# Optimization experiments

Hardware: AMD Instinct MI355X
Metric: run time of the kernel (lower is better)

Reference implementation:

```python
import jax, jax.numpy as jnp
import numpy as np

N, D_IN, D_OUT = 8192, 256, 64
NEG_INF = -9e15
LEAKY_SLOPE = 0.2  # tf.nn.leaky_relu default alpha


def setup_inputs() -> dict:
    key = jax.random.key(0)
    k1, k2, k3, k4 = jax.random.split(key, 4)
    x = jax.random.normal(k1, (N, D_IN), dtype=jnp.float32)
    adj = jax.random.randint(k2, (N, N), 0, 2, dtype=jnp.int32)
    W = jax.random.normal(k3, (D_IN, D_OUT), dtype=jnp.float32) * (1.0 / np.sqrt(D_IN))
    a = jax.random.normal(k4, (2 * D_OUT, 1), dtype=jnp.float32) * (1.0 / np.sqrt(2 * D_OUT))
    b = jnp.zeros((D_OUT,), dtype=jnp.float32)
    return {"x": x, "adj": adj, "W": W, "a": a, "b": b}


def reference(x, adj, W, a, b):
    # z: [N, D_OUT]
    z = x @ W
    # Additive GAT scores: e[i,j] = leaky_relu(a1.z_i + a2.z_j)
    # (equivalent to the tile/concat + matmul with a in the original,
    #  but avoids the [N*N, 2D] intermediate)
    a1 = a[:D_OUT, 0]   # [D_OUT]
    a2 = a[D_OUT:, 0]   # [D_OUT]
    si = z @ a1         # [N]
    sj = z @ a2         # [N]
    e = jax.nn.leaky_relu(si[:, None] + sj[None, :], negative_slope=LEAKY_SLOPE)
    masked = jnp.where(adj > 0, e, NEG_INF)
    alpha = jax.nn.softmax(masked, axis=1)  # row-wise over neighbors
    out = alpha @ z + b
    return jax.nn.relu(out)
```

## Files before the change

### kernel.cpp

```cpp
#include <hip/hip_runtime.h>
#include <hip/hip_bf16.h>

#define N 8192
#define DIN 256
#define DOUT 64
#define JSPLIT 16
#define JSPAN (N / JSPLIT)
#define NITILES (N / 64)
#define LEAKY 0.2f

typedef __attribute__((ext_vector_type(8))) short bf16x8;
typedef __attribute__((ext_vector_type(4))) float f32x4;

#define OFF_ZT   ((size_t)0)
#define OFF_SI   (OFF_ZT + (size_t)DOUT * N * 2)
#define OFF_SJ   (OFF_SI + (size_t)N * 4)
#define OFF_MAX  (OFF_SJ + (size_t)N * 4)
#define OFF_PDEN (OFF_MAX + 256)
#define OFF_PNUM (OFF_PDEN + (size_t)JSPLIT * N * 4)

static __device__ __forceinline__ short f2bf(float f) {
  union { __hip_bfloat16 h; short s; } u;
  u.h = __float2bfloat16(f);
  return u.s;
}

static __device__ __forceinline__ unsigned fkey(float f) {
  int b = __float_as_int(f);
  return (b < 0) ? ~(unsigned)b : ((unsigned)b | 0x80000000u);
}
static __device__ __forceinline__ float fdec(unsigned k) {
  int b = (k & 0x80000000u) ? (int)(k & 0x7fffffffu) : (int)~k;
  return __int_as_float(b);
}

__global__ __launch_bounds__(256) void gat_proj(
    const float* __restrict__ x, const float* __restrict__ W,
    const float* __restrict__ a, __hip_bfloat16* __restrict__ zT,
    float* __restrict__ si, float* __restrict__ sj,
    unsigned* __restrict__ mx) {
  __shared__ float wmx[4][2];
  const int lane = threadIdx.x & 63;
  const int wave = threadIdx.x >> 6;
  const int rowbase = blockIdx.x * 16 + wave * 4;
  float acc[4] = {0.f, 0.f, 0.f, 0.f};
  for (int k = 0; k < DIN; k += 4) {
    const float w0 = W[(k + 0) * DOUT + lane];
    const float w1 = W[(k + 1) * DOUT + lane];
    const float w2 = W[(k + 2) * DOUT + lane];
    const float w3 = W[(k + 3) * DOUT + lane];
#pragma unroll
    for (int r = 0; r < 4; ++r) {
      const float4 xv = *reinterpret_cast<const float4*>(&x[(size_t)(rowbase + r) * DIN + k]);
      acc[r] += xv.x * w0 + xv.y * w1 + xv.z * w2 + xv.w * w3;
    }
  }
  const float a1l = a[lane];
  const float a2l = a[DOUT + lane];
  float wm1 = -1e30f, wm2 = -1e30f;
#pragma unroll
  for (int r = 0; r < 4; ++r) {
    const int row = rowbase + r;
    zT[(size_t)lane * N + row] = __float2bfloat16(acc[r]);
    float v1 = acc[r] * a1l;
    float v2 = acc[r] * a2l;
#pragma unroll
    for (int m = 1; m < 64; m <<= 1) {
      v1 += __shfl_xor(v1, m);
      v2 += __shfl_xor(v2, m);
    }
    if (lane == 0) { si[row] = v1; sj[row] = v2; }
    wm1 = fmaxf(wm1, v1);
    wm2 = fmaxf(wm2, v2);
  }
  if (lane == 0) { wmx[wave][0] = wm1; wmx[wave][1] = wm2; }
  __syncthreads();
  if (threadIdx.x == 0) {
    float M1 = fmaxf(fmaxf(wmx[0][0], wmx[1][0]), fmaxf(wmx[2][0], wmx[3][0]));
    float M2 = fmaxf(fmaxf(wmx[0][1], wmx[1][1]), fmaxf(wmx[2][1], wmx[3][1]));
    atomicMax(mx + 0, fkey(M1));
    atomicMax(mx + 1, fkey(M2));
  }
}

__global__ __launch_bounds__(256, 6) void gat_main(
    const int* __restrict__ adj, const float* __restrict__ si,
    const float* __restrict__ sj, const __hip_bfloat16* __restrict__ zT,
    const unsigned* __restrict__ mx, float* __restrict__ pnum,
    float* __restrict__ pden) {
  const int lane = threadIdx.x & 63;
  const int wave = threadIdx.x >> 6;
  const int itile = blockIdx.x % NITILES;
  const int jchunk = blockIdx.x / NITILES;
  const int r16 = lane & 15;
  const int kgrp = lane >> 4;
  const int row = itile * 64 + wave * 16 + r16;
  const int jbase = jchunk * JSPAN;

  unsigned bm0 = 0, bm1 = 0, bm2 = 0, bm3 = 0;
  {
    const int* __restrict__ abase =
        adj + (size_t)(itile * 64 + wave * 16) * N + jbase;
#pragma unroll 1
    for (int rr = 0; rr < 16; ++rr) {
      const int* __restrict__ ar = abase + (size_t)rr * N;
#pragma unroll
      for (int w = 0; w < 8; ++w) {
        const int v = ar[w * 64 + lane];
        const unsigned long long m = __ballot(v > 0);
        const unsigned byte0 = (unsigned)(m >> (kgrp * 8)) & 0xffu;
        const unsigned byte1 = (unsigned)(m >> (32 + kgrp * 8)) & 0xffu;
        const unsigned contrib = (byte0 | (byte1 << 8)) << ((w & 1) * 16);
        if (r16 == rr) {
          if ((w >> 1) == 0) bm0 |= contrib;
          else if ((w >> 1) == 1) bm1 |= contrib;
          else if ((w >> 1) == 2) bm2 |= contrib;
          else bm3 |= contrib;
        }
      }
    }
  }

  const float tC = fdec(mx[0]) + fdec(mx[1]);
  const float C = tC > 0.f ? tC : LEAKY * tC;
  const float sir = si[row];

  const float* __restrict__ sp = sj + jbase + kgrp * 8;
  const __hip_bfloat16* __restrict__ zb0 = zT + (size_t)r16 * N + jbase + kgrp * 8;
  const __hip_bfloat16* __restrict__ zb1 = zb0 + (size_t)16 * N;
  const __hip_bfloat16* __restrict__ zb2 = zb0 + (size_t)32 * N;
  const __hip_bfloat16* __restrict__ zb3 = zb0 + (size_t)48 * N;

  f32x4 acc0 = {0.f, 0.f, 0.f, 0.f};
  f32x4 acc1 = acc0, acc2 = acc0, acc3 = acc0;
  float dacc = 0.f;

#pragma unroll
  for (int ph = 0; ph < 4; ++ph) {
    const unsigned bmp = (ph == 0) ? bm0 : (ph == 1) ? bm1 : (ph == 2) ? bm2 : bm3;
#pragma unroll
    for (int sub = 0; sub < 4; ++sub) {
      const int it = ph * 4 + sub;
      const unsigned bits = (bmp >> (sub * 8)) & 0xffu;

      const bf16x8 b0 = *reinterpret_cast<const bf16x8*>(zb0 + it * 32);
      const bf16x8 b1 = *reinterpret_cast<const bf16x8*>(zb1 + it * 32);
      const bf16x8 b2 = *reinterpret_cast<const bf16x8*>(zb2 + it * 32);
      const bf16x8 b3 = *reinterpret_cast<const bf16x8*>(zb3 + it * 32);
      const float4 s0 = *reinterpret_cast<const float4*>(sp + it * 32);
      const float4 s1 = *reinterpret_cast<const float4*>(sp + it * 32 + 4);

      float p0, p1, p2, p3, p4, p5, p6, p7, t;
      t = sir + s0.x; t = fmaxf(t, LEAKY * t); p0 = (bits & 1u)   ? __expf(t - C) : 0.f;
      t = sir + s0.y; t = fmaxf(t, LEAKY * t); p1 = (bits & 2u)   ? __expf(t - C) : 0.f;
      t = sir + s0.z; t = fmaxf(t, LEAKY * t); p2 = (bits & 4u)   ? __expf(t - C) : 0.f;
      t = sir + s0.w; t = fmaxf(t, LEAKY * t); p3 = (bits & 8u)   ? __expf(t - C) : 0.f;
      t = sir + s1.x; t = fmaxf(t, LEAKY * t); p4 = (bits & 16u)  ? __expf(t - C) : 0.f;
      t = sir + s1.y; t = fmaxf(t, LEAKY * t); p5 = (bits & 32u)  ? __expf(t - C) : 0.f;
      t = sir + s1.z; t = fmaxf(t, LEAKY * t); p6 = (bits & 64u)  ? __expf(t - C) : 0.f;
      t = sir + s1.w; t = fmaxf(t, LEAKY * t); p7 = (bits & 128u) ? __expf(t - C) : 0.f;

      dacc += ((p0 + p1) + (p2 + p3)) + ((p4 + p5) + (p6 + p7));

      bf16x8 afr;
      afr[0] = f2bf(p0); afr[1] = f2bf(p1); afr[2] = f2bf(p2); afr[3] = f2bf(p3);
      afr[4] = f2bf(p4); afr[5] = f2bf(p5); afr[6] = f2bf(p6); afr[7] = f2bf(p7);

      acc0 = __builtin_amdgcn_mfma_f32_16x16x32_bf16(afr, b0, acc0, 0, 0, 0);
      acc1 = __builtin_amdgcn_mfma_f32_16x16x32_bf16(afr, b1, acc1, 0, 0, 0);
      acc2 = __builtin_amdgcn_mfma_f32_16x16x32_bf16(afr, b2, acc2, 0, 0, 0);
      acc3 = __builtin_amdgcn_mfma_f32_16x16x32_bf16(afr, b3, acc3, 0, 0, 0);
    }
  }

  dacc += __shfl_xor(dacc, 16);
  dacc += __shfl_xor(dacc, 32);
  if (lane < 16) pden[(size_t)jchunk * N + row] = dacc;

  float* np = pnum + ((size_t)jchunk * N + (size_t)itile * 64 + wave * 16) * DOUT;
  const f32x4 accs[4] = {acc0, acc1, acc2, acc3};
#pragma unroll
  for (int dt = 0; dt < 4; ++dt) {
#pragma unroll
    for (int r = 0; r < 4; ++r) {
      np[(kgrp * 4 + r) * DOUT + dt * 16 + r16] = accs[dt][r];
    }
  }
}

__global__ __launch_bounds__(256) void gat_combine(
    const float* __restrict__ pnum, const float* __restrict__ pden,
    const float* __restrict__ b, float* __restrict__ out) {
  const int idx = blockIdx.x * 256 + threadIdx.x;
  const int row = idx >> 6;
  const int d = idx & 63;
  float num = 0.f, den = 0.f;
#pragma unroll
  for (int s = 0; s < JSPLIT; ++s) num += pnum[(size_t)s * N * DOUT + idx];
#pragma unroll
  for (int s = 0; s < JSPLIT; ++s) den += pden[(size_t)s * N + row];
  const float o = num / den + b[d];
  out[idx] = o > 0.f ? o : 0.f;
}

extern "C" void kernel_launch(void* const* d_in, const int* in_sizes, int n_in,
                              void* d_out, int out_size, void* d_ws, size_t ws_size,
                              hipStream_t stream) {
  const float* x = (const float*)d_in[0];
  const int* adj = (const int*)d_in[1];
  const float* W = (const float*)d_in[2];
  const float* a = (const float*)d_in[3];
  const float* b = (const float*)d_in[4];
  float* out = (float*)d_out;
  char* ws = (char*)d_ws;

  __hip_bfloat16* zT = (__hip_bfloat16*)(ws + OFF_ZT);
  float* si = (float*)(ws + OFF_SI);
  float* sj = (float*)(ws + OFF_SJ);
  unsigned* mx = (unsigned*)(ws + OFF_MAX);
  float* pden = (float*)(ws + OFF_PDEN);
  float* pnum = (float*)(ws + OFF_PNUM);

  gat_proj<<<dim3(N / 16), dim3(256), 0, stream>>>(x, W, a, zT, si, sj, mx);
  gat_main<<<dim3(NITILES * JSPLIT), dim3(256), 0, stream>>>(adj, si, sj, zT, mx,
                                                             pnum, pden);
  gat_combine<<<dim3((N * DOUT) / 256), dim3(256), 0, stream>>>(pnum, pden, b, out);
}
```

Baseline: 480.9 us.

## Stage z tile in LDS and split j range into 32 chunks

```diff
diff --git a/kernel.cpp b/kernel.cpp
--- a/kernel.cpp
+++ b/kernel.cpp
@@ -4,8 +4,9 @@
 #define N 8192
 #define DIN 256
 #define DOUT 64
-#define JSPLIT 16
+#define JSPLIT 32
 #define JSPAN (N / JSPLIT)
+#define KSTEPS (JSPAN / 32)
 #define NITILES (N / 64)
 #define LEAKY 0.2f
 
@@ -83,13 +84,15 @@
   }
 }
 
-__global__ __launch_bounds__(256, 6) void gat_main(
+__global__ __launch_bounds__(256, 4) void gat_main(
     const int* __restrict__ adj, const float* __restrict__ si,
     const float* __restrict__ sj, const __hip_bfloat16* __restrict__ zT,
     const unsigned* __restrict__ mx, float* __restrict__ pnum,
     float* __restrict__ pden) {
-  const int lane = threadIdx.x & 63;
-  const int wave = threadIdx.x >> 6;
+  __shared__ short lds_z[64][264];
+  const int tid = threadIdx.x;
+  const int lane = tid & 63;
+  const int wave = tid >> 6;
   const int itile = blockIdx.x % NITILES;
   const int jchunk = blockIdx.x / NITILES;
   const int r16 = lane & 15;
@@ -97,80 +100,81 @@
   const int row = itile * 64 + wave * 16 + r16;
   const int jbase = jchunk * JSPAN;
 
-  unsigned bm0 = 0, bm1 = 0, bm2 = 0, bm3 = 0;
+  {
+    const int r = tid >> 5;
+    const int cb = (tid & 31) * 8;
+#pragma unroll
+    for (int rr = 0; rr < 8; ++rr) {
+      const int d = rr * 8 + r;
+      const bf16x8 v =
+          *reinterpret_cast<const bf16x8*>(zT + (size_t)d * N + jbase + cb);
+      *reinterpret_cast<bf16x8*>(&lds_z[d][cb]) = v;
+    }
+  }
+
+  unsigned bm0 = 0, bm1 = 0;
   {
     const int* __restrict__ abase =
         adj + (size_t)(itile * 64 + wave * 16) * N + jbase;
-#pragma unroll 1
+#pragma unroll
     for (int rr = 0; rr < 16; ++rr) {
-      const int* __restrict__ ar = abase + (size_t)rr * N;
-#pragma unroll
-      for (int w = 0; w < 8; ++w) {
-        const int v = ar[w * 64 + lane];
+#pragma unroll
+      for (int w = 0; w < 4; ++w) {
+        const int v = abase[(size_t)rr * N + w * 64 + lane];
         const unsigned long long m = __ballot(v > 0);
         const unsigned byte0 = (unsigned)(m >> (kgrp * 8)) & 0xffu;
         const unsigned byte1 = (unsigned)(m >> (32 + kgrp * 8)) & 0xffu;
         const unsigned contrib = (byte0 | (byte1 << 8)) << ((w & 1) * 16);
         if (r16 == rr) {
-          if ((w >> 1) == 0) bm0 |= contrib;
-          else if ((w >> 1) == 1) bm1 |= contrib;
-          else if ((w >> 1) == 2) bm2 |= contrib;
-          else bm3 |= contrib;
+          if (w < 2) bm0 |= contrib; else bm1 |= contrib;
         }
       }
     }
   }
+  __syncthreads();
 
   const float tC = fdec(mx[0]) + fdec(mx[1]);
   const float C = tC > 0.f ? tC : LEAKY * tC;
   const float sir = si[row];
-
   const float* __restrict__ sp = sj + jbase + kgrp * 8;
-  const __hip_bfloat16* __restrict__ zb0 = zT + (size_t)r16 * N + jbase + kgrp * 8;
-  const __hip_bfloat16* __restrict__ zb1 = zb0 + (size_t)16 * N;
-  const __hip_bfloat16* __restrict__ zb2 = zb0 + (size_t)32 * N;
-  const __hip_bfloat16* __restrict__ zb3 = zb0 + (size_t)48 * N;
 
   f32x4 acc0 = {0.f, 0.f, 0.f, 0.f};
   f32x4 acc1 = acc0, acc2 = acc0, acc3 = acc0;
   float dacc = 0.f;
 
 #pragma unroll
-  for (int ph = 0; ph < 4; ++ph) {
-    const unsigned bmp = (ph == 0) ? bm0 : (ph == 1) ? bm1 : (ph == 2) ? bm2 : bm3;
-#pragma unroll
-    for (int sub = 0; sub < 4; ++sub) {
-      const int it = ph * 4 + sub;
-      const unsigned bits = (bmp >> (sub * 8)) & 0xffu;
-
-      const bf16x8 b0 = *reinterpret_cast<const bf16x8*>(zb0 + it * 32);
-      const bf16x8 b1 = *reinterpret_cast<const bf16x8*>(zb1 + it * 32);
-      const bf16x8 b2 = *reinterpret_cast<const bf16x8*>(zb2 + it * 32);
-      const bf16x8 b3 = *reinterpret_cast<const bf16x8*>(zb3 + it * 32);
-      const float4 s0 = *reinterpret_cast<const float4*>(sp + it * 32);
-      const float4 s1 = *reinterpret_cast<const float4*>(sp + it * 32 + 4);
-
-      float p0, p1, p2, p3, p4, p5, p6, p7, t;
-      t = sir + s0.x; t = fmaxf(t, LEAKY * t); p0 = (bits & 1u)   ? __expf(t - C) : 0.f;
-      t = sir + s0.y; t = fmaxf(t, LEAKY * t); p1 = (bits & 2u)   ? __expf(t - C) : 0.f;
-      t = sir + s0.z; t = fmaxf(t, LEAKY * t); p2 = (bits & 4u)   ? __expf(t - C) : 0.f;
-      t = sir + s0.w; t = fmaxf(t, LEAKY * t); p3 = (bits & 8u)   ? __expf(t - C) : 0.f;
-      t = sir + s1.x; t = fmaxf(t, LEAKY * t); p4 = (bits & 16u)  ? __expf(t - C) : 0.f;
-      t = sir + s1.y; t = fmaxf(t, LEAKY * t); p5 = (bits & 32u)  ? __expf(t - C) : 0.f;
-      t = sir + s1.z; t = fmaxf(t, LEAKY * t); p6 = (bits & 64u)  ? __expf(t - C) : 0.f;
-      t = sir + s1.w; t = fmaxf(t, LEAKY * t); p7 = (bits & 128u) ? __expf(t - C) : 0.f;
-
-      dacc += ((p0 + p1) + (p2 + p3)) + ((p4 + p5) + (p6 + p7));
-
-      bf16x8 afr;
-      afr[0] = f2bf(p0); afr[1] = f2bf(p1); afr[2] = f2bf(p2); afr[3] = f2bf(p3);
-      afr[4] = f2bf(p4); afr[5] = f2bf(p5); afr[6] = f2bf(p6); afr[7] = f2bf(p7);
-
-      acc0 = __builtin_amdgcn_mfma_f32_16x16x32_bf16(afr, b0, acc0, 0, 0, 0);
-      acc1 = __builtin_amdgcn_mfma_f32_16x16x32_bf16(afr, b1, acc1, 0, 0, 0);
-      acc2 = __builtin_amdgcn_mfma_f32_16x16x32_bf16(afr, b2, acc2, 0, 0, 0);
-      acc3 = __builtin_amdgcn_mfma_f32_16x16x32_bf16(afr, b3, acc3, 0, 0, 0);
-    }
+  for (int it = 0; it < KSTEPS; ++it) {
+    const unsigned bmp = (it < 4) ? bm0 : bm1;
+    const unsigned bits = (bmp >> ((it & 3) * 8)) & 0xffu;
+    const int col = it * 32 + kgrp * 8;
+
+    const bf16x8 b0 = *reinterpret_cast<const bf16x8*>(&lds_z[r16][col]);
+    const bf16x8 b1 = *reinterpret_cast<const bf16x8*>(&lds_z[16 + r16][col]);
+    const bf16x8 b2 = *reinterpret_cast<const bf16x8*>(&lds_z[32 + r16][col]);
+    const bf16x8 b3 = *reinterpret_cast<const bf16x8*>(&lds_z[48 + r16][col]);
+    const float4 s0 = *reinterpret_cast<const float4*>(sp + it * 32);
+    const float4 s1 = *reinterpret_cast<const float4*>(sp + it * 32 + 4);
+
+    float p0, p1, p2, p3, p4, p5, p6, p7, t;
+    t = sir + s0.x; t = fmaxf(t, LEAKY * t); p0 = (bits & 1u)   ? __expf(t - C) : 0.f;
+    t = sir + s0.y; t = fmaxf(t, LEAKY * t); p1 = (bits & 2u)   ? __expf(t - C) : 0.f;
+    t = sir + s0.z; t = fmaxf(t, LEAKY * t); p2 = (bits & 4u)   ? __expf(t - C) : 0.f;
+    t = sir + s0.w; t = fmaxf(t, LEAKY * t); p3 = (bits & 8u)   ? __expf(t - C) : 0.f;
+    t = sir + s1.x; t = fmaxf(t, LEAKY * t); p4 = (bits & 16u)  ? __expf(t - C) : 0.f;
+    t = sir + s1.y; t = fmaxf(t, LEAKY * t); p5 = (bits & 32u)  ? __expf(t - C) : 0.f;
+    t = sir + s1.z; t = fmaxf(t, LEAKY * t); p6 = (bits & 64u)  ? __expf(t - C) : 0.f;
+    t = sir + s1.w; t = fmaxf(t, LEAKY * t); p7 = (bits & 128u) ? __expf(t - C) : 0.f;
+
+    dacc += ((p0 + p1) + (p2 + p3)) + ((p4 + p5) + (p6 + p7));
+
+    bf16x8 afr;
+    afr[0] = f2bf(p0); afr[1] = f2bf(p1); afr[2] = f2bf(p2); afr[3] = f2bf(p3);
+    afr[4] = f2bf(p4); afr[5] = f2bf(p5); afr[6] = f2bf(p6); afr[7] = f2bf(p7);
+
+    acc0 = __builtin_amdgcn_mfma_f32_16x16x32_bf16(afr, b0, acc0, 0, 0, 0);
+    acc1 = __builtin_amdgcn_mfma_f32_16x16x32_bf16(afr, b1, acc1, 0, 0, 0);
+    acc2 = __builtin_amdgcn_mfma_f32_16x16x32_bf16(afr, b2, acc2, 0, 0, 0);
+    acc3 = __builtin_amdgcn_mfma_f32_16x16x32_bf16(afr, b3, acc3, 0, 0, 0);
   }
 
   dacc += __shfl_xor(dacc, 16);
```

After: 438.4 us. -8.8%, faster.
